# Optimization experiments

Hardware: AMD Instinct MI355X
Metric: run time of the kernel (lower is better)

Reference implementation:

```python
import jax, jax.numpy as jnp
import numpy as np

H, HS, NH, T = 2048, 64, 32, 1024
DD, DA, DG, DV = 64, 64, 128, 32


def _ln(x, w, b, eps):
    mu = x.mean(-1, keepdims=True)
    var = ((x - mu) ** 2).mean(-1, keepdims=True)
    return (x - mu) / jnp.sqrt(var + eps) * w + b


def setup_inputs() -> dict:
    key = jax.random.key(0)
    ks = jax.random.split(key, 40)
    n = lambda i, shape, s=0.02: (jax.random.normal(ks[i], shape, jnp.float32) * s)
    u = lambda i, shape: jax.random.uniform(ks[i], shape, jnp.float32)
    return {
        'x': jax.random.normal(ks[0], (1, T, H), jnp.float32),
        'state1': jax.random.normal(ks[1], (1, H), jnp.float32),
        'state2': jnp.zeros((NH, HS, HS), jnp.float32),
        'v_first': jax.random.normal(ks[2], (1, T, H), jnp.float32),
        'x_r': u(3, (H,)), 'x_w': u(4, (H,)), 'x_k': u(5, (H,)),
        'x_v': u(6, (H,)), 'x_a': u(7, (H,)), 'x_g': u(8, (H,)),
        'W_r': n(9, (H, H)), 'W_k': n(10, (H, H)), 'W_v': n(11, (H, H)), 'W_o': n(12, (H, H)),
        'w0': n(13, (H,), 0.5) - 0.6,
        'w1': n(14, (H, DD)), 'w2': n(15, (DD, H)),
        'a0': jnp.zeros((H,), jnp.float32), 'a1': n(16, (H, DA)), 'a2': n(17, (DA, H)),
        'v0': jnp.zeros((H,), jnp.float32), 'v1': n(18, (H, DV)), 'v2': n(19, (DV, H)),
        'g1': n(20, (H, DG)), 'g2': n(21, (DG, H)),
        'k_k': n(22, (NH, HS), 0.5) + 1.0, 'k_a': n(23, (NH, HS), 0.5) + 1.0,
        'r_k': n(24, (NH, HS), 0.5),
        'ln_x_w': jnp.ones((H,), jnp.float32), 'ln_x_b': jnp.zeros((H,), jnp.float32),
        'ln1_w': jnp.ones((H,), jnp.float32), 'ln1_b': jnp.zeros((H,), jnp.float32),
    }


def reference(x, state1, state2, v_first, x_r, x_w, x_k, x_v, x_a, x_g,
              W_r, W_k, W_v, W_o, w0, w1, w2, a0, a1, a2, v0, v1, v2,
              g1, g2, k_k, k_a, r_k, ln_x_w, ln_x_b, ln1_w, ln1_b):
    T = x.shape[1]
    NH, HS = k_k.shape
    Hd = NH * HS
    last_x = x
    xn = _ln(x, ln1_w, ln1_b, 1e-5)
    # token shift: sx = shifted_past - x
    past = jnp.concatenate([state1[:, None, :], xn[:, :-1, :]], axis=1)
    sx = past - xn
    state1_out = xn[:, -1, :]
    xr = xn + x_r * sx
    xw = xn + x_w * sx
    xk = xn + x_k * sx
    xv = xn + x_v * sx
    xa = xn + x_a * sx
    xg = xn + x_g * sx
    r = xr @ W_r.T                                  # [1,T,H]
    k = (xk @ W_k.T).reshape(T, NH, HS)
    v = xv @ W_v.T                                  # [1,T,H]
    g = jax.nn.sigmoid(xg @ g1) @ g2                # gate
    a = jax.nn.sigmoid(a0 + (xa @ a1) @ a2).reshape(T, NH, HS)
    w = jnp.tanh(xw @ w1) @ w2                      # decay LoRA
    kk = k * k_k
    kk = kk / (jnp.linalg.norm(kk, axis=-1, keepdims=True) + 1e-12)
    k = k * (1.0 + (a - 1.0) * k_a)
    # layer_id != 0: v residual toward v_first
    v = v + (v_first - v) * jax.nn.sigmoid(v0 + (xv @ v1) @ v2)
    w = jnp.exp(-0.606531 * jax.nn.sigmoid(w0 + w)).reshape(T, NH, HS)
    b_seq = kk * a        # in-context addition direction
    a_seq = -kk           # removal direction
    r3 = r.reshape(T, NH, HS)
    v3 = v.reshape(T, NH, HS)

    def step(S, ts):
        w_t, k_t, v_t, a_t, b_t, r_t = ts          # each [NH,HS]
        S = S * w_t[:, None, :]                     # column-wise decay
        sa = jnp.einsum('hij,hj->hi', S, a_t)       # S @ a
        S = S + sa[:, :, None] * b_t[:, None, :] + v_t[:, :, None] * k_t[:, None, :]
        out = jnp.einsum('hij,hj->hi', S, r_t)      # S @ r
        return S, out

    state2_out, y = jax.lax.scan(step, state2, (w, k, v3, a_seq, b_seq, r3))  # y: [T,NH,HS]
    y = _ln(y, 1.0, 0.0, 0.00064)                   # GroupNorm-style per-head LN (no affine)
    y = y.reshape(1, T, Hd) * ln_x_w + ln_x_b
    bonus = ((r3 * k * r_k).sum(-1, keepdims=True) * v3).reshape(1, T, Hd)
    y = (y + bonus) * g
    y = y @ W_o.T
    return (last_x + y, state1_out, state2_out, v_first)
```

## Files before the change

### kernel.cpp

```cpp
#include <hip/hip_runtime.h>
#include <hip/hip_bf16.h>
#include <cstdint>
#include <cstddef>

#define T_TOK 1024
#define H_DIM 2048
#define NH 32
#define HS 64
#define TH (T_TOK * H_DIM)
#define HH (H_DIM * H_DIM)

using short8 = __attribute__((ext_vector_type(8))) short;
using f32x4  = __attribute__((ext_vector_type(4))) float;
using i32x4  = __attribute__((ext_vector_type(4))) int;
typedef __hip_bfloat16 bf16;

__device__ __forceinline__ float sigmoidf_(float x) { return 1.0f / (1.0f + expf(-x)); }

__device__ __forceinline__ float wsum64(float v) {
#pragma unroll
    for (int m = 32; m; m >>= 1) v += __shfl_xor(v, m, 64);
    return v;
}

__device__ __forceinline__ float dpp_add16(float x) {
    int t;
    t = __builtin_amdgcn_update_dpp(0, __float_as_int(x), 0xB1, 0xF, 0xF, true);
    x += __int_as_float(t);
    t = __builtin_amdgcn_update_dpp(0, __float_as_int(x), 0x4E, 0xF, 0xF, true);
    x += __int_as_float(t);
    t = __builtin_amdgcn_update_dpp(0, __float_as_int(x), 0x141, 0xF, 0xF, true);
    x += __int_as_float(t);
    t = __builtin_amdgcn_update_dpp(0, __float_as_int(x), 0x140, 0xF, 0xF, true);
    x += __int_as_float(t);
    return x;
}

struct CastPar { const float* src[4]; bf16* dst[4]; };
__global__ __launch_bounds__(256) void castw_kernel(CastPar p) {
    int z = blockIdx.z;
    const float4* s = (const float4*)p.src[z];
    bf16* d = p.dst[z];
    int i = blockIdx.x * 256 + threadIdx.x;
    float4 v = s[i];
    int b = i * 4;
    d[b + 0] = __float2bfloat16(v.x);
    d[b + 1] = __float2bfloat16(v.y);
    d[b + 2] = __float2bfloat16(v.z);
    d[b + 3] = __float2bfloat16(v.w);
}

struct TPar { const float* src[8]; bf16* dst[8]; int R[8]; int C[8]; };
__global__ __launch_bounds__(256) void transpose_kernel(TPar p) {
    int z = blockIdx.z;
    int R = p.R[z], C = p.C[z];
    int e = blockIdx.x * 256 + threadIdx.x;
    if (e >= R * C) return;
    int r = e / C, c = e % C;
    p.dst[z][(size_t)c * R + r] = __float2bfloat16(p.src[z][e]);
}

__global__ __launch_bounds__(256) void ln_kernel(const float* __restrict__ x,
                                                 const float* __restrict__ w,
                                                 const float* __restrict__ b,
                                                 float* __restrict__ xn,
                                                 float* __restrict__ s1out) {
    int t = blockIdx.x, tid = threadIdx.x;
    const float* xt = x + (size_t)t * H_DIM;
    float v[8]; float s = 0.f, s2 = 0.f;
#pragma unroll
    for (int e = 0; e < 8; e++) { v[e] = xt[tid + 256 * e]; s += v[e]; s2 += v[e] * v[e]; }
    s = wsum64(s); s2 = wsum64(s2);
    __shared__ float ls[8];
    int wid = tid >> 6, ln = tid & 63;
    if (ln == 0) { ls[wid] = s; ls[4 + wid] = s2; }
    __syncthreads();
    s = ls[0] + ls[1] + ls[2] + ls[3];
    s2 = ls[4] + ls[5] + ls[6] + ls[7];
    float mu = s * (1.f / H_DIM);
    float var = s2 * (1.f / H_DIM) - mu * mu;
    float inv = rsqrtf(var + 1e-5f);
#pragma unroll
    for (int e = 0; e < 8; e++) {
        int h = tid + 256 * e;
        float o = (v[e] - mu) * inv * w[h] + b[h];
        xn[(size_t)t * H_DIM + h] = o;
        if (t == T_TOK - 1) s1out[h] = o;
    }
}

struct MixPar { const float* xn; const float* state1; const float* mv[6]; bf16* out[6]; };
__global__ __launch_bounds__(256) void mix_kernel(MixPar p) {
    int t = blockIdx.x, tid = threadIdx.x;
#pragma unroll
    for (int e = 0; e < 8; e++) {
        int h = tid + 256 * e;
        size_t idx = (size_t)t * H_DIM + h;
        float cur = p.xn[idx];
        float prev = (t == 0) ? p.state1[h] : p.xn[idx - H_DIM];
        float sx = prev - cur;
#pragma unroll
        for (int q = 0; q < 6; q++)
            p.out[q][idx] = __float2bfloat16(cur + p.mv[q][h] * sx);
    }
}

typedef const __attribute__((address_space(1))) uint32_t* gp1_t;
typedef __attribute__((address_space(3))) uint32_t* lp3_t;
__device__ __forceinline__ void async16(const bf16* g, short* l) {
    __builtin_amdgcn_global_load_lds((gp1_t)g, (lp3_t)l, 16, 0, 0);
}

struct BGPar { const bf16* X[4]; const bf16* W[4]; float* out[4]; const float* resid[4]; };
__global__ __launch_bounds__(256) void bgemm_kernel(BGPar p) {
    int z = blockIdx.z;
    const bf16* __restrict__ X = p.X[z];
    const bf16* __restrict__ W = p.W[z];
    float* __restrict__ out = p.out[z];
    const float* __restrict__ resid = p.resid[z];

    __shared__ short As[4][128 * 32];
    __shared__ short Bs[4][128 * 32];

    int m0 = blockIdx.y * 128, n0 = blockIdx.x * 128;
    int tid = threadIdx.x, lane = tid & 63, wv = tid >> 6;
    int m_off = (wv >> 1) * 64, n_off = (wv & 1) * 64;
    int lr = lane & 15, lq = lane >> 4;

    int srow = lane >> 2;
    int scol = (lane & 3) * 8;
    const bf16* Ag0 = X + (size_t)(m0 + wv * 32 + srow) * 2048 + scol;
    const bf16* Ag1 = Ag0 + (size_t)16 * 2048;
    const bf16* Bg0 = W + (size_t)(n0 + wv * 32 + srow) * 2048 + scol;
    const bf16* Bg1 = Bg0 + (size_t)16 * 2048;

    auto issue = [&](int at, int nb) {
        int kk = at * 32;
        async16(Ag0 + kk, &As[nb][(wv * 32) * 32]);
        async16(Ag1 + kk, &As[nb][(wv * 32 + 16) * 32]);
        async16(Bg0 + kk, &Bs[nb][(wv * 32) * 32]);
        async16(Bg1 + kk, &Bs[nb][(wv * 32 + 16) * 32]);
    };

    f32x4 acc[4][4];
#pragma unroll
    for (int a = 0; a < 4; a++)
#pragma unroll
        for (int b = 0; b < 4; b++)
#pragma unroll
            for (int r = 0; r < 4; r++) acc[a][b][r] = 0.f;

    issue(0, 0); issue(1, 1); issue(2, 2);

    for (int it = 0; it < 64; it++) {
        int nt = it + 3;
        int at = nt > 63 ? 63 : nt;
        issue(at, nt & 3);
        asm volatile("s_waitcnt vmcnt(12)" ::: "memory");
        asm volatile("s_barrier" ::: "memory");
        int buf = it & 3;
        short8 af[4], bfr[4];
#pragma unroll
        for (int mi = 0; mi < 4; mi++)
            af[mi] = *(const short8*)&As[buf][(m_off + mi * 16 + lr) * 32 + lq * 8];
#pragma unroll
        for (int ni = 0; ni < 4; ni++)
            bfr[ni] = *(const short8*)&Bs[buf][(n_off + ni * 16 + lr) * 32 + lq * 8];
#pragma unroll
        for (int mi = 0; mi < 4; mi++)
#pragma unroll
            for (int ni = 0; ni < 4; ni++)
                acc[mi][ni] = __builtin_amdgcn_mfma_f32_16x16x32_bf16(af[mi], bfr[ni], acc[mi][ni], 0, 0, 0);
        asm volatile("s_barrier" ::: "memory");
    }
    asm volatile("s_waitcnt vmcnt(0)" ::: "memory");

#pragma unroll
    for (int mi = 0; mi < 4; mi++)
#pragma unroll
        for (int ni = 0; ni < 4; ni++)
#pragma unroll
            for (int r = 0; r < 4; r++) {
                int rowg = m0 + m_off + mi * 16 + lq * 4 + r;
                int colg = n0 + n_off + ni * 16 + lr;
                size_t o = (size_t)rowg * 2048 + colg;
                float v = acc[mi][ni][r];
                if (resid) v += resid[o];
                out[o] = v;
            }
}

#define BM 128
#define BN 128
#define BK 32
#define LDK 40

__device__ __forceinline__ void gemm_core(const bf16* __restrict__ X, const bf16* __restrict__ W,
                                          int M, int N, int K, int act,
                                          const float* __restrict__ bias,
                                          float* __restrict__ outF, bf16* __restrict__ outB) {
    __shared__ short As[BM * LDK];
    __shared__ short Bs[BN * LDK];
    int m0 = blockIdx.y * BM, n0 = blockIdx.x * BN;
    if (n0 >= N) return;
    int tid = threadIdx.x;
    int lane = tid & 63, wid = tid >> 6;
    int m_off = (wid >> 1) * 64, n_off = (wid & 1) * 64;
    int lr = lane & 15, lq = lane >> 4;

    f32x4 acc[4][4];
#pragma unroll
    for (int a = 0; a < 4; a++)
#pragma unroll
        for (int b = 0; b < 4; b++)
#pragma unroll
            for (int r = 0; r < 4; r++) acc[a][b][r] = 0.f;

    for (int k0 = 0; k0 < K; k0 += BK) {
#pragma unroll
        for (int it = 0; it < 2; it++) {
            int c = tid + it * 256;
            int r = c >> 2;
            int cc = (c & 3) * 8;
            uint4 va = *(const uint4*)(X + (size_t)(m0 + r) * K + k0 + cc);
            *(uint4*)&As[r * LDK + cc] = va;
            uint4 vb;
            if (n0 + r < N) vb = *(const uint4*)(W + (size_t)(n0 + r) * K + k0 + cc);
            else            vb = make_uint4(0u, 0u, 0u, 0u);
            *(uint4*)&Bs[r * LDK + cc] = vb;
        }
        __syncthreads();
        short8 af[4], bfr[4];
#pragma unroll
        for (int mi = 0; mi < 4; mi++)
            af[mi] = *(const short8*)&As[(m_off + mi * 16 + lr) * LDK + lq * 8];
#pragma unroll
        for (int ni = 0; ni < 4; ni++)
            bfr[ni] = *(const short8*)&Bs[(n_off + ni * 16 + lr) * LDK + lq * 8];
#pragma unroll
        for (int mi = 0; mi < 4; mi++)
#pragma unroll
            for (int ni = 0; ni < 4; ni++)
                acc[mi][ni] = __builtin_amdgcn_mfma_f32_16x16x32_bf16(af[mi], bfr[ni], acc[mi][ni], 0, 0, 0);
        __syncthreads();
    }
#pragma unroll
    for (int mi = 0; mi < 4; mi++)
#pragma unroll
        for (int ni = 0; ni < 4; ni++)
#pragma unroll
            for (int r = 0; r < 4; r++) {
                int rowg = m0 + m_off + mi * 16 + lq * 4 + r;
                int colg = n0 + n_off + ni * 16 + lr;
                if (colg < N) {
                    float v = acc[mi][ni][r];
                    if (bias) v += bias[colg];
                    if (act == 1) v = sigmoidf_(v);
                    else if (act == 2) v = tanhf(v);
                    size_t o = (size_t)rowg * N + colg;
                    if (outF) outF[o] = v;
                    else      outB[o] = __float2bfloat16(v);
                }
            }
}

struct GPar {
    const bf16* X[4]; const bf16* W[4];
    float* outF[4]; bf16* outB[4];
    const float* bias[4];
    int N[4]; int K[4]; int act[4]; int M;
};
__global__ __launch_bounds__(256) void gemm_z_kernel(GPar p) {
    int z = blockIdx.z;
    gemm_core(p.X[z], p.W[z], p.M, p.N[z], p.K[z], p.act[z], p.bias[z], p.outF[z], p.outB[z]);
}

__global__ __launch_bounds__(64) void prep_kernel(float* __restrict__ k_io, float* __restrict__ v_io,
                                                  const float* __restrict__ v_first,
                                                  const float* __restrict__ vres,
                                                  float* __restrict__ w_io,
                                                  const float* __restrict__ a_io,
                                                  const float* __restrict__ r_in,
                                                  bf16* __restrict__ pk,
                                                  const float* __restrict__ k_k,
                                                  const float* __restrict__ k_a,
                                                  const float* __restrict__ w0) {
    int h = blockIdx.x, t = blockIdx.y, i = threadIdx.x;
    int hi = h * HS + i;
    size_t idx = (size_t)t * H_DIM + hi;
    float kf = k_io[idx];
    float kk = kf * k_k[hi];
    float ss = wsum64(kk * kk);
    float kkn = kk / (sqrtf(ss) + 1e-12f);
    float a = a_io[idx];
    float knew = kf * (1.f + (a - 1.f) * k_a[hi]);
    k_io[idx] = knew;
    float vv = v_io[idx];
    v_io[idx] = vv + (v_first[idx] - vv) * vres[idx];
    w_io[idx] = expf(-0.606531f * sigmoidf_(w0[hi] + w_io[idx]));
    size_t pb = (((size_t)t * NH + h) * 16 + (i >> 2)) * 16 + (i & 3);
    pk[pb + 0]  = __float2bfloat16(-kkn);
    pk[pb + 4]  = __float2bfloat16(kkn * a);
    pk[pb + 8]  = __float2bfloat16(knew);
    pk[pb + 12] = __float2bfloat16(r_in[idx]);
}

struct SlotV { f32x4 w; i32x4 q0, q1; float v; };

#define SCAN_ISSUE(sl, tt)                                                              \
    do {                                                                                \
        int tc_ = (tt) < T_TOK ? (tt) : T_TOK - 1;                                      \
        const float* wp_ = w_s + (size_t)tc_ * H_DIM + hb;                              \
        const bf16*  pp_ = pk + (size_t)tc_ * (NH * 256) + h * 256;                     \
        const float* vp_ = v_s + (size_t)tc_ * H_DIM + hb;                              \
        asm volatile("global_load_dwordx4 %0, %1, %2" : "=v"((sl).w) : "v"(jow), "s"(wp_)); \
        asm volatile("global_load_dwordx4 %0, %1, %2" : "=v"((sl).q0) : "v"(pko), "s"(pp_)); \
        asm volatile("global_load_dwordx4 %0, %1, %2 offset:16" : "=v"((sl).q1) : "v"(pko), "s"(pp_)); \
        asm volatile("global_load_dword %0, %1, %2" : "=v"((sl).v) : "v"(rowoff), "s"(vp_)); \
    } while (0)

#define SCAN_PIN(sl)                                                                    \
    asm volatile("" : "+v"((sl).w), "+v"((sl).q0), "+v"((sl).q1), "+v"((sl).v))

__device__ __forceinline__ void scan_compute(float S[4], const SlotV& s,
                                             const float* __restrict__ yp, int rowoff) {
    float af[4], bb[4], kf[4], rf[4];
    uint32_t u;
    u = (uint32_t)s.q0[0]; af[0] = __uint_as_float(u << 16); af[1] = __uint_as_float(u & 0xffff0000u);
    u = (uint32_t)s.q0[1]; af[2] = __uint_as_float(u << 16); af[3] = __uint_as_float(u & 0xffff0000u);
    u = (uint32_t)s.q0[2]; bb[0] = __uint_as_float(u << 16); bb[1] = __uint_as_float(u & 0xffff0000u);
    u = (uint32_t)s.q0[3]; bb[2] = __uint_as_float(u << 16); bb[3] = __uint_as_float(u & 0xffff0000u);
    u = (uint32_t)s.q1[0]; kf[0] = __uint_as_float(u << 16); kf[1] = __uint_as_float(u & 0xffff0000u);
    u = (uint32_t)s.q1[1]; kf[2] = __uint_as_float(u << 16); kf[3] = __uint_as_float(u & 0xffff0000u);
    u = (uint32_t)s.q1[2]; rf[0] = __uint_as_float(u << 16); rf[1] = __uint_as_float(u & 0xffff0000u);
    u = (uint32_t)s.q1[3]; rf[2] = __uint_as_float(u << 16); rf[3] = __uint_as_float(u & 0xffff0000u);
    float sa = 0.f;
#pragma unroll
    for (int e = 0; e < 4; e++) { S[e] *= s.w[e]; sa = fmaf(S[e], af[e], sa); }
    sa = dpp_add16(sa);
    float o = 0.f;
#pragma unroll
    for (int e = 0; e < 4; e++) {
        S[e] = fmaf(sa, bb[e], fmaf(s.v, kf[e], S[e]));
        o = fmaf(S[e], rf[e], o);
    }
    o = dpp_add16(o);
    asm volatile("global_store_dword %0, %1, %2" :: "v"(rowoff), "v"(o), "s"(yp) : "memory");
}

#define SCAN_STEP(d, t, W)                                                              \
    do {                                                                                \
        asm volatile("s_waitcnt vmcnt(" W ")");                                         \
        SCAN_PIN(sv[d]);                                                                \
        scan_compute(S, sv[d], y + (size_t)(t) * H_DIM + hb, rowoff);                   \
        SCAN_ISSUE(sv[d], (t) + 4);                                                     \
    } while (0)

__global__ __launch_bounds__(64) void scan_kernel(const float* __restrict__ w_s,
                                                  const bf16* __restrict__ pk,
                                                  const float* __restrict__ v_s,
                                                  const float* __restrict__ s2in,
                                                  float* __restrict__ y,
                                                  float* __restrict__ s2out) {
    int h = blockIdx.x, q = blockIdx.y;
    int lane = threadIdx.x;
    int il = lane >> 4, jb = lane & 15;
    int row = q * 4 + il;
    int jo = jb * 4;
    int hb = h * HS;
    int jow = jo * 4;
    int pko = jb * 32;
    int rowoff = row * 4;

    float S[4];
    {
        const float* s0 = s2in + (size_t)h * HS * HS + (size_t)row * HS + jo;
        float4 t0 = *(const float4*)s0;
        S[0] = t0.x; S[1] = t0.y; S[2] = t0.z; S[3] = t0.w;
    }

    SlotV sv[4];
    SCAN_ISSUE(sv[0], 0);
    SCAN_ISSUE(sv[1], 1);
    SCAN_ISSUE(sv[2], 2);
    SCAN_ISSUE(sv[3], 3);

    SCAN_STEP(0, 0, "12");
    SCAN_STEP(1, 1, "13");
    SCAN_STEP(2, 2, "14");
    SCAN_STEP(3, 3, "15");
    for (int tb = 4; tb < T_TOK; tb += 4) {
        SCAN_STEP(0, tb + 0, "15");
        SCAN_STEP(1, tb + 1, "15");
        SCAN_STEP(2, tb + 2, "15");
        SCAN_STEP(3, tb + 3, "15");
    }
    asm volatile("s_waitcnt vmcnt(0)" ::: "memory");

    {
        float* so = s2out + (size_t)h * HS * HS + (size_t)row * HS + jo;
        float4 t0;
        t0.x = S[0]; t0.y = S[1]; t0.z = S[2]; t0.w = S[3];
        *(float4*)so = t0;
    }
}

__global__ __launch_bounds__(64) void post_kernel(const float* __restrict__ y,
                                                  const float* __restrict__ r_s,
                                                  const float* __restrict__ k_s,
                                                  const float* __restrict__ v_s,
                                                  const float* __restrict__ g_s,
                                                  const float* __restrict__ r_k,
                                                  const float* __restrict__ lnw,
                                                  const float* __restrict__ lnb,
                                                  bf16* __restrict__ ybig) {
    int h = blockIdx.x, t = blockIdx.y, i = threadIdx.x;
    int hi = h * HS + i;
    size_t idx = (size_t)t * H_DIM + hi;
    float yv = y[idx];
    float mu = wsum64(yv) * (1.f / HS);
    float d = yv - mu;
    float var = wsum64(d * d) * (1.f / HS);
    float yn = d * rsqrtf(var + 0.00064f);
    float bd = wsum64(r_s[idx] * k_s[idx] * r_k[hi]);
    float val = (yn * lnw[hi] + lnb[hi] + bd * v_s[idx]) * g_s[idx];
    ybig[idx] = __float2bfloat16(val);
}

extern "C" void kernel_launch(void* const* d_in, const int* in_sizes, int n_in,
                              void* d_out, int out_size, void* d_ws, size_t ws_size,
                              hipStream_t stream) {
    const float* x      = (const float*)d_in[0];
    const float* state1 = (const float*)d_in[1];
    const float* state2 = (const float*)d_in[2];
    const float* vfirst = (const float*)d_in[3];
    const float* x_r = (const float*)d_in[4];
    const float* x_w = (const float*)d_in[5];
    const float* x_k = (const float*)d_in[6];
    const float* x_v = (const float*)d_in[7];
    const float* x_a = (const float*)d_in[8];
    const float* x_g = (const float*)d_in[9];
    const float* W_r = (const float*)d_in[10];
    const float* W_k = (const float*)d_in[11];
    const float* W_v = (const float*)d_in[12];
    const float* W_o = (const float*)d_in[13];
    const float* w0 = (const float*)d_in[14];
    const float* w1 = (const float*)d_in[15];
    const float* w2 = (const float*)d_in[16];
    const float* a0 = (const float*)d_in[17];
    const float* a1 = (const float*)d_in[18];
    const float* a2 = (const float*)d_in[19];
    const float* v0 = (const float*)d_in[20];
    const float* v1 = (const float*)d_in[21];
    const float* v2 = (const float*)d_in[22];
    const float* g1 = (const float*)d_in[23];
    const float* g2 = (const float*)d_in[24];
    const float* k_k = (const float*)d_in[25];
    const float* k_a = (const float*)d_in[26];
    const float* r_k = (const float*)d_in[27];
    const float* ln_x_w = (const float*)d_in[28];
    const float* ln_x_b = (const float*)d_in[29];
    const float* ln1_w = (const float*)d_in[30];
    const float* ln1_b = (const float*)d_in[31];

    float* out0 = (float*)d_out;
    float* out1 = out0 + TH;
    float* out2 = out1 + H_DIM;
    float* out3 = out2 + NH * HS * HS;

    float* F = (float*)d_ws;
    float* xn   = F;
    float* rb   = F + (size_t)1 * TH;
    float* kb   = F + (size_t)2 * TH;
    float* vb   = F + (size_t)3 * TH;
    float* ab   = F + (size_t)4 * TH;
    float* wpre = F + (size_t)5 * TH;
    float* vresb= F + (size_t)6 * TH;
    float* gb   = F + (size_t)7 * TH;
    float* yb   = F + (size_t)8 * TH;
    bf16* B = (bf16*)(F + (size_t)9 * TH);
    bf16 *xrb = B, *xwb = B + (size_t)TH, *xkb = B + (size_t)2 * TH,
         *xvb = B + (size_t)3 * TH, *xab = B + (size_t)4 * TH, *xgb = B + (size_t)5 * TH;
    bf16* Wrb = B + (size_t)6 * TH;
    bf16* Wkb = Wrb + (size_t)HH;
    bf16* Wvb = Wkb + (size_t)HH;
    bf16* Wob = Wvb + (size_t)HH;
    bf16* pp = Wob + (size_t)HH;
    bf16* a1T = pp; pp += (size_t)H_DIM * 64;
    bf16* w1T = pp; pp += (size_t)H_DIM * 64;
    bf16* v1T = pp; pp += (size_t)H_DIM * 32;
    bf16* g1T = pp; pp += (size_t)H_DIM * 128;
    bf16* a2T = pp; pp += (size_t)H_DIM * 64;
    bf16* w2T = pp; pp += (size_t)H_DIM * 64;
    bf16* v2T = pp; pp += (size_t)H_DIM * 32;
    bf16* g2T = pp; pp += (size_t)H_DIM * 128;
    bf16* amid = pp; pp += (size_t)T_TOK * 64;
    bf16* wmid = pp; pp += (size_t)T_TOK * 64;
    bf16* vmid = pp; pp += (size_t)T_TOK * 32;
    bf16* gmid = pp; pp += (size_t)T_TOK * 128;
    bf16* ybig = pp; pp += (size_t)TH;

    bf16* PK = Wrb;

    CastPar cp;
    cp.src[0] = W_r; cp.src[1] = W_k; cp.src[2] = W_v; cp.src[3] = W_o;
    cp.dst[0] = Wrb; cp.dst[1] = Wkb; cp.dst[2] = Wvb; cp.dst[3] = Wob;
    castw_kernel<<<dim3(HH / 4 / 256, 1, 4), 256, 0, stream>>>(cp);

    TPar tp;
    tp.src[0] = a1; tp.dst[0] = a1T; tp.R[0] = H_DIM; tp.C[0] = 64;
    tp.src[1] = w1; tp.dst[1] = w1T; tp.R[1] = H_DIM; tp.C[1] = 64;
    tp.src[2] = v1; tp.dst[2] = v1T; tp.R[2] = H_DIM; tp.C[2] = 32;
    tp.src[3] = g1; tp.dst[3] = g1T; tp.R[3] = H_DIM; tp.C[3] = 128;
    tp.src[4] = a2; tp.dst[4] = a2T; tp.R[4] = 64;  tp.C[4] = H_DIM;
    tp.src[5] = w2; tp.dst[5] = w2T; tp.R[5] = 64;  tp.C[5] = H_DIM;
    tp.src[6] = v2; tp.dst[6] = v2T; tp.R[6] = 32;  tp.C[6] = H_DIM;
    tp.src[7] = g2; tp.dst[7] = g2T; tp.R[7] = 128; tp.C[7] = H_DIM;
    transpose_kernel<<<dim3((H_DIM * 128 + 255) / 256, 1, 8), 256, 0, stream>>>(tp);

    ln_kernel<<<dim3(T_TOK), 256, 0, stream>>>(x, ln1_w, ln1_b, xn, out1);

    MixPar mp; mp.xn = xn; mp.state1 = state1;
    mp.mv[0] = x_r; mp.mv[1] = x_w; mp.mv[2] = x_k; mp.mv[3] = x_v; mp.mv[4] = x_a; mp.mv[5] = x_g;
    mp.out[0] = xrb; mp.out[1] = xwb; mp.out[2] = xkb; mp.out[3] = xvb; mp.out[4] = xab; mp.out[5] = xgb;
    mix_kernel<<<dim3(T_TOK), 256, 0, stream>>>(mp);

    BGPar bp{};
    bp.X[0] = xrb; bp.W[0] = Wrb; bp.out[0] = rb; bp.resid[0] = nullptr;
    bp.X[1] = xkb; bp.W[1] = Wkb; bp.out[1] = kb; bp.resid[1] = nullptr;
    bp.X[2] = xvb; bp.W[2] = Wvb; bp.out[2] = vb; bp.resid[2] = nullptr;
    bgemm_kernel<<<dim3(16, 8, 3), 256, 0, stream>>>(bp);

    GPar s1{}; s1.M = T_TOK;
    s1.X[0] = xab; s1.W[0] = a1T; s1.outB[0] = amid; s1.N[0] = 64;  s1.K[0] = H_DIM; s1.act[0] = 0;
    s1.X[1] = xwb; s1.W[1] = w1T; s1.outB[1] = wmid; s1.N[1] = 64;  s1.K[1] = H_DIM; s1.act[1] = 2;
    s1.X[2] = xvb; s1.W[2] = v1T; s1.outB[2] = vmid; s1.N[2] = 32;  s1.K[2] = H_DIM; s1.act[2] = 0;
    s1.X[3] = xgb; s1.W[3] = g1T; s1.outB[3] = gmid; s1.N[3] = 128; s1.K[3] = H_DIM; s1.act[3] = 1;
    gemm_z_kernel<<<dim3(1, 8, 4), 256, 0, stream>>>(s1);

    GPar s2{}; s2.M = T_TOK;
    s2.X[0] = amid; s2.W[0] = a2T; s2.outF[0] = ab;    s2.N[0] = H_DIM; s2.K[0] = 64;  s2.act[0] = 1; s2.bias[0] = a0;
    s2.X[1] = wmid; s2.W[1] = w2T; s2.outF[1] = wpre;  s2.N[1] = H_DIM; s2.K[1] = 64;  s2.act[1] = 0;
    s2.X[2] = vmid; s2.W[2] = v2T; s2.outF[2] = vresb; s2.N[2] = H_DIM; s2.K[2] = 32;  s2.act[2] = 1; s2.bias[2] = v0;
    s2.X[3] = gmid; s2.W[3] = g2T; s2.outF[3] = gb;    s2.N[3] = H_DIM; s2.K[3] = 128; s2.act[3] = 0;
    gemm_z_kernel<<<dim3(16, 8, 4), 256, 0, stream>>>(s2);

    prep_kernel<<<dim3(NH, T_TOK), 64, 0, stream>>>(kb, vb, vfirst, vresb, wpre, ab, rb, PK, k_k, k_a, w0);

    scan_kernel<<<dim3(NH, 16), 64, 0, stream>>>(wpre, PK, vb, state2, yb, out2);

    post_kernel<<<dim3(NH, T_TOK), 64, 0, stream>>>(yb, rb, kb, vb, gb, r_k, ln_x_w, ln_x_b, ybig);

    BGPar bo{};
    bo.X[0] = ybig; bo.W[0] = Wob; bo.out[0] = out0; bo.resid[0] = x;
    bgemm_kernel<<<dim3(16, 8, 1), 256, 0, stream>>>(bo);

    hipMemcpyAsync(out3, (const void*)vfirst, (size_t)TH * sizeof(float),
                   hipMemcpyDeviceToDevice, stream);
}
```

Baseline: 593.6 us.

## Stage scan inputs through LDS with a dedicated loader wave and head-major records

Prep now writes per-head, token-contiguous 768-byte records (w, a/b, k/r packed) plus a head-major v buffer, so each chunk of tokens is one contiguous block. The scan kernel uses 3 waves: one issues async global-to-LDS loads four chunks deep, and two compute waves read w/a/b/k/r/v from shared memory after a barrier each chunk. This replaces per-wave register-prefetched global loads with bulk contiguous transfers, shared across two waves handling 8 rows. It adds a block barrier per 8 tokens and halves the grid's y dimension.

```diff
diff --git a/kernel.cpp b/kernel.cpp
--- a/kernel.cpp
+++ b/kernel.cpp
@@ -108,6 +108,9 @@
 typedef const __attribute__((address_space(1))) uint32_t* gp1_t;
 typedef __attribute__((address_space(3))) uint32_t* lp3_t;
 __device__ __forceinline__ void async16(const bf16* g, short* l) {
+    __builtin_amdgcn_global_load_lds((gp1_t)g, (lp3_t)l, 16, 0, 0);
+}
+__device__ __forceinline__ void async16v(const void* g, void* l) {
     __builtin_amdgcn_global_load_lds((gp1_t)g, (lp3_t)l, 16, 0, 0);
 }
 
@@ -278,10 +281,11 @@
 __global__ __launch_bounds__(64) void prep_kernel(float* __restrict__ k_io, float* __restrict__ v_io,
                                                   const float* __restrict__ v_first,
                                                   const float* __restrict__ vres,
-                                                  float* __restrict__ w_io,
+                                                  const float* __restrict__ w_in,
                                                   const float* __restrict__ a_io,
                                                   const float* __restrict__ r_in,
-                                                  bf16* __restrict__ pk,
+                                                  char* __restrict__ pkw,
+                                                  float* __restrict__ vh,
                                                   const float* __restrict__ k_k,
                                                   const float* __restrict__ k_a,
                                                   const float* __restrict__ w0) {
@@ -296,109 +300,111 @@
     float knew = kf * (1.f + (a - 1.f) * k_a[hi]);
     k_io[idx] = knew;
     float vv = v_io[idx];
-    v_io[idx] = vv + (v_first[idx] - vv) * vres[idx];
-    w_io[idx] = expf(-0.606531f * sigmoidf_(w0[hi] + w_io[idx]));
-    size_t pb = (((size_t)t * NH + h) * 16 + (i >> 2)) * 16 + (i & 3);
-    pk[pb + 0]  = __float2bfloat16(-kkn);
-    pk[pb + 4]  = __float2bfloat16(kkn * a);
-    pk[pb + 8]  = __float2bfloat16(knew);
-    pk[pb + 12] = __float2bfloat16(r_in[idx]);
-}
-
-struct SlotV { f32x4 w; i32x4 q0, q1; float v; };
-
-#define SCAN_ISSUE(sl, tt)                                                              \
-    do {                                                                                \
-        int tc_ = (tt) < T_TOK ? (tt) : T_TOK - 1;                                      \
-        const float* wp_ = w_s + (size_t)tc_ * H_DIM + hb;                              \
-        const bf16*  pp_ = pk + (size_t)tc_ * (NH * 256) + h * 256;                     \
-        const float* vp_ = v_s + (size_t)tc_ * H_DIM + hb;                              \
-        asm volatile("global_load_dwordx4 %0, %1, %2" : "=v"((sl).w) : "v"(jow), "s"(wp_)); \
-        asm volatile("global_load_dwordx4 %0, %1, %2" : "=v"((sl).q0) : "v"(pko), "s"(pp_)); \
-        asm volatile("global_load_dwordx4 %0, %1, %2 offset:16" : "=v"((sl).q1) : "v"(pko), "s"(pp_)); \
-        asm volatile("global_load_dword %0, %1, %2" : "=v"((sl).v) : "v"(rowoff), "s"(vp_)); \
-    } while (0)
-
-#define SCAN_PIN(sl)                                                                    \
-    asm volatile("" : "+v"((sl).w), "+v"((sl).q0), "+v"((sl).q1), "+v"((sl).v))
-
-__device__ __forceinline__ void scan_compute(float S[4], const SlotV& s,
-                                             const float* __restrict__ yp, int rowoff) {
-    float af[4], bb[4], kf[4], rf[4];
-    uint32_t u;
-    u = (uint32_t)s.q0[0]; af[0] = __uint_as_float(u << 16); af[1] = __uint_as_float(u & 0xffff0000u);
-    u = (uint32_t)s.q0[1]; af[2] = __uint_as_float(u << 16); af[3] = __uint_as_float(u & 0xffff0000u);
-    u = (uint32_t)s.q0[2]; bb[0] = __uint_as_float(u << 16); bb[1] = __uint_as_float(u & 0xffff0000u);
-    u = (uint32_t)s.q0[3]; bb[2] = __uint_as_float(u << 16); bb[3] = __uint_as_float(u & 0xffff0000u);
-    u = (uint32_t)s.q1[0]; kf[0] = __uint_as_float(u << 16); kf[1] = __uint_as_float(u & 0xffff0000u);
-    u = (uint32_t)s.q1[1]; kf[2] = __uint_as_float(u << 16); kf[3] = __uint_as_float(u & 0xffff0000u);
-    u = (uint32_t)s.q1[2]; rf[0] = __uint_as_float(u << 16); rf[1] = __uint_as_float(u & 0xffff0000u);
-    u = (uint32_t)s.q1[3]; rf[2] = __uint_as_float(u << 16); rf[3] = __uint_as_float(u & 0xffff0000u);
-    float sa = 0.f;
-#pragma unroll
-    for (int e = 0; e < 4; e++) { S[e] *= s.w[e]; sa = fmaf(S[e], af[e], sa); }
-    sa = dpp_add16(sa);
-    float o = 0.f;
-#pragma unroll
-    for (int e = 0; e < 4; e++) {
-        S[e] = fmaf(sa, bb[e], fmaf(s.v, kf[e], S[e]));
-        o = fmaf(S[e], rf[e], o);
-    }
-    o = dpp_add16(o);
-    asm volatile("global_store_dword %0, %1, %2" :: "v"(rowoff), "v"(o), "s"(yp) : "memory");
-}
-
-#define SCAN_STEP(d, t, W)                                                              \
-    do {                                                                                \
-        asm volatile("s_waitcnt vmcnt(" W ")");                                         \
-        SCAN_PIN(sv[d]);                                                                \
-        scan_compute(S, sv[d], y + (size_t)(t) * H_DIM + hb, rowoff);                   \
-        SCAN_ISSUE(sv[d], (t) + 4);                                                     \
-    } while (0)
-
-__global__ __launch_bounds__(64) void scan_kernel(const float* __restrict__ w_s,
-                                                  const bf16* __restrict__ pk,
-                                                  const float* __restrict__ v_s,
-                                                  const float* __restrict__ s2in,
-                                                  float* __restrict__ y,
-                                                  float* __restrict__ s2out) {
-    int h = blockIdx.x, q = blockIdx.y;
-    int lane = threadIdx.x;
+    float vnew = vv + (v_first[idx] - vv) * vres[idx];
+    v_io[idx] = vnew;
+    float wfin = expf(-0.606531f * sigmoidf_(w0[hi] + w_in[idx]));
+
+    char* rec = pkw + ((size_t)h * T_TOK + t) * 768;
+    ((float*)rec)[i] = wfin;
+    int sub = (i >> 2) * 8 + (i & 3);
+    bf16* ab = (bf16*)(rec + 256);
+    bf16* kr = (bf16*)(rec + 512);
+    ab[sub]     = __float2bfloat16(-kkn);
+    ab[sub + 4] = __float2bfloat16(kkn * a);
+    kr[sub]     = __float2bfloat16(knew);
+    kr[sub + 4] = __float2bfloat16(r_in[idx]);
+
+    vh[((size_t)h * T_TOK + t) * HS + i] = vnew;
+}
+
+#define SC_CH 8
+#define SC_SLOT 8192
+__global__ __launch_bounds__(192) void scan_kernel(const char* __restrict__ pkw,
+                                                   const float* __restrict__ vh,
+                                                   const float* __restrict__ s2in,
+                                                   float* __restrict__ y,
+                                                   float* __restrict__ s2out) {
+    __shared__ char smem[4 * SC_SLOT];
+    int h = blockIdx.x, bq = blockIdx.y;
+    int wid = threadIdx.x >> 6;
+    int lane = threadIdx.x & 63;
+    int hb = h * HS;
+
+    int q = bq * 2 + wid;
     int il = lane >> 4, jb = lane & 15;
     int row = q * 4 + il;
-    int jo = jb * 4;
-    int hb = h * HS;
-    int jow = jo * 4;
-    int pko = jb * 32;
-    int rowoff = row * 4;
-
-    float S[4];
-    {
-        const float* s0 = s2in + (size_t)h * HS * HS + (size_t)row * HS + jo;
+
+    float S[4] = {0.f, 0.f, 0.f, 0.f};
+    if (wid < 2) {
+        const float* s0 = s2in + (size_t)h * HS * HS + (size_t)row * HS + (size_t)jb * 4;
         float4 t0 = *(const float4*)s0;
         S[0] = t0.x; S[1] = t0.y; S[2] = t0.z; S[3] = t0.w;
     }
 
-    SlotV sv[4];
-    SCAN_ISSUE(sv[0], 0);
-    SCAN_ISSUE(sv[1], 1);
-    SCAN_ISSUE(sv[2], 2);
-    SCAN_ISSUE(sv[3], 3);
-
-    SCAN_STEP(0, 0, "12");
-    SCAN_STEP(1, 1, "13");
-    SCAN_STEP(2, 2, "14");
-    SCAN_STEP(3, 3, "15");
-    for (int tb = 4; tb < T_TOK; tb += 4) {
-        SCAN_STEP(0, tb + 0, "15");
-        SCAN_STEP(1, tb + 1, "15");
-        SCAN_STEP(2, tb + 2, "15");
-        SCAN_STEP(3, tb + 3, "15");
-    }
-    asm volatile("s_waitcnt vmcnt(0)" ::: "memory");
-
-    {
-        float* so = s2out + (size_t)h * HS * HS + (size_t)row * HS + jo;
+    auto issue_chunk = [&](int c) {
+        char* lb = smem + (size_t)(c & 3) * SC_SLOT;
+        const char* gp = pkw + ((size_t)h * T_TOK + (size_t)c * SC_CH) * 768;
+        const char* gv = (const char*)vh + ((size_t)h * T_TOK + (size_t)c * SC_CH) * 256;
+#pragma unroll
+        for (int i = 0; i < 6; i++)
+            async16v(gp + i * 1024 + lane * 16, lb + i * 1024);
+#pragma unroll
+        for (int i = 0; i < 2; i++)
+            async16v(gv + i * 1024 + lane * 16, lb + 6144 + i * 1024);
+    };
+
+    if (wid == 2) {
+        issue_chunk(0); issue_chunk(1); issue_chunk(2);
+    }
+
+    for (int c = 0; c < T_TOK / SC_CH; c++) {
+        if (wid == 2)
+            asm volatile("s_waitcnt vmcnt(16)" ::: "memory");
+        asm volatile("" ::: "memory");
+        __builtin_amdgcn_s_barrier();
+        asm volatile("" ::: "memory");
+        if (wid == 2) {
+            int cn = c + 3;
+            if (cn > T_TOK / SC_CH - 1) cn = T_TOK / SC_CH - 1;
+            issue_chunk(cn);
+        } else {
+            const char* lb = smem + (size_t)(c & 3) * SC_SLOT;
+#pragma unroll
+            for (int j = 0; j < SC_CH; j++) {
+                int t = c * SC_CH + j;
+                f32x4 wv = *(const f32x4*)(lb + j * 768 + jb * 16);
+                i32x4 q0 = *(const i32x4*)(lb + j * 768 + 256 + jb * 16);
+                i32x4 q1 = *(const i32x4*)(lb + j * 768 + 512 + jb * 16);
+                float vvv = *(const float*)(lb + 6144 + j * 256 + row * 4);
+                float af[4], bb[4], kf[4], rf[4];
+                uint32_t u;
+                u = (uint32_t)q0[0]; af[0] = __uint_as_float(u << 16); af[1] = __uint_as_float(u & 0xffff0000u);
+                u = (uint32_t)q0[1]; af[2] = __uint_as_float(u << 16); af[3] = __uint_as_float(u & 0xffff0000u);
+                u = (uint32_t)q0[2]; bb[0] = __uint_as_float(u << 16); bb[1] = __uint_as_float(u & 0xffff0000u);
+                u = (uint32_t)q0[3]; bb[2] = __uint_as_float(u << 16); bb[3] = __uint_as_float(u & 0xffff0000u);
+                u = (uint32_t)q1[0]; kf[0] = __uint_as_float(u << 16); kf[1] = __uint_as_float(u & 0xffff0000u);
+                u = (uint32_t)q1[1]; kf[2] = __uint_as_float(u << 16); kf[3] = __uint_as_float(u & 0xffff0000u);
+                u = (uint32_t)q1[2]; rf[0] = __uint_as_float(u << 16); rf[1] = __uint_as_float(u & 0xffff0000u);
+                u = (uint32_t)q1[3]; rf[2] = __uint_as_float(u << 16); rf[3] = __uint_as_float(u & 0xffff0000u);
+                float sa = 0.f;
+#pragma unroll
+                for (int e = 0; e < 4; e++) { S[e] *= wv[e]; sa = fmaf(S[e], af[e], sa); }
+                sa = dpp_add16(sa);
+                float o = 0.f;
+#pragma unroll
+                for (int e = 0; e < 4; e++) {
+                    S[e] = fmaf(sa, bb[e], fmaf(vvv, kf[e], S[e]));
+                    o = fmaf(S[e], rf[e], o);
+                }
+                o = dpp_add16(o);
+                y[(size_t)t * H_DIM + hb + row] = o;
+            }
+        }
+    }
+    if (wid == 2) {
+        asm volatile("s_waitcnt vmcnt(0)" ::: "memory");
+    } else {
+        float* so = s2out + (size_t)h * HS * HS + (size_t)row * HS + (size_t)jb * 4;
         float4 t0;
         t0.x = S[0]; t0.y = S[1]; t0.z = S[2]; t0.w = S[3];
         *(float4*)so = t0;
@@ -500,7 +506,8 @@
     bf16* gmid = pp; pp += (size_t)T_TOK * 128;
     bf16* ybig = pp; pp += (size_t)TH;
 
-    bf16* PK = Wrb;
+    char* PKW = (char*)Wrb;
+    float* VH = xn;
 
     CastPar cp;
     cp.src[0] = W_r; cp.src[1] = W_k; cp.src[2] = W_v; cp.src[3] = W_o;
@@ -545,9 +552,9 @@
     s2.X[3] = gmid; s2.W[3] = g2T; s2.outF[3] = gb;    s2.N[3] = H_DIM; s2.K[3] = 128; s2.act[3] = 0;
     gemm_z_kernel<<<dim3(16, 8, 4), 256, 0, stream>>>(s2);
 
-    prep_kernel<<<dim3(NH, T_TOK), 64, 0, stream>>>(kb, vb, vfirst, vresb, wpre, ab, rb, PK, k_k, k_a, w0);
-
-    scan_kernel<<<dim3(NH, 16), 64, 0, stream>>>(wpre, PK, vb, state2, yb, out2);
+    prep_kernel<<<dim3(NH, T_TOK), 64, 0, stream>>>(kb, vb, vfirst, vresb, wpre, ab, rb, PKW, VH, k_k, k_a, w0);
+
+    scan_kernel<<<dim3(NH, 8), 192, 0, stream>>>(PKW, VH, state2, yb, out2);
 
     post_kernel<<<dim3(NH, T_TOK), 64, 0, stream>>>(yb, rb, kb, vb, gb, r_k, ln_x_w, ln_x_b, ybig);
 
```

Result: no change. 588.0 us (-0.9%).
